# Kernel tuning notes

Measured on AMD Instinct MI355X. Metric: run time of the kernel, lower is better.

The kernel has to match this reference:

```python
import jax, jax.numpy as jnp
import numpy as np

IMG_W, IMG_H = 128, 128
N_PTS = 256
MIN_D, MAX_D = 2.0, 6.0
FOCAL = 1.7320508  # 1/tan(fov/2), fov=60deg (FoVPerspectiveCameras default)
SCALING = 0.1      # scaling_factor default
EPS_EA = 1e-10     # pytorch3d EmissionAbsorptionRaymarcher eps


def setup_inputs() -> dict:
    key = jax.random.key(0)
    k1, k2 = jax.random.split(key)
    image3d = jax.random.uniform(k1, (1, 1, 128, 128, 128), jnp.float32)
    opacity = jax.random.uniform(k2, (1, 1, 128, 128, 128), jnp.float32)
    # row-vector camera convention (pytorch3d): p_cam = p_world @ R + T
    R = jnp.zeros((1, 3, 3), jnp.float32).at[:, jnp.arange(3), jnp.arange(3)].set(1.0)
    T = jnp.zeros((1, 3), jnp.float32).at[:, 2].set(4.0)
    return {"image3d": image3d, "opacity": opacity, "R": R, "T": T}


def _trilinear(vol, pts):
    """vol [C,D,H,W]; pts [N,3] xyz in [-1,1] (x->W, y->H, z->D).
    align_corners=True, zero padding outside. Returns [N,C]."""
    C, D, H, W = vol.shape
    x = (pts[:, 0] + 1.0) * 0.5 * (W - 1)
    y = (pts[:, 1] + 1.0) * 0.5 * (H - 1)
    z = (pts[:, 2] + 1.0) * 0.5 * (D - 1)
    x0 = jnp.floor(x); y0 = jnp.floor(y); z0 = jnp.floor(z)
    wx = x - x0; wy = y - y0; wz = z - z0
    vol_flat = vol.reshape(C, -1)
    out = jnp.zeros((pts.shape[0], C), vol.dtype)
    for dz in (0, 1):
        for dy in (0, 1):
            for dx in (0, 1):
                xi = (x0 + dx).astype(jnp.int32)
                yi = (y0 + dy).astype(jnp.int32)
                zi = (z0 + dz).astype(jnp.int32)
                valid = ((xi >= 0) & (xi < W) & (yi >= 0) & (yi < H)
                         & (zi >= 0) & (zi < D))
                w = ((wx if dx else 1.0 - wx) * (wy if dy else 1.0 - wy)
                     * (wz if dz else 1.0 - wz)) * valid.astype(vol.dtype)
                idx = ((jnp.clip(zi, 0, D - 1) * H + jnp.clip(yi, 0, H - 1)) * W
                       + jnp.clip(xi, 0, W - 1))
                vals = jnp.take(vol_flat, idx, axis=1)  # [C,N]
                out = out + w[:, None] * vals.T
    return out


def _forward(image3d, opacity, R, T):
    B = image3d.shape[0]
    features_vol = jnp.repeat(image3d, 3, axis=1)            # [B,3,D,H,W]
    densities_vol = opacity * SCALING                        # [B,1,D,H,W]
    Dv, Hv, Wv = image3d.shape[2:]
    shape = max(image3d.shape[1], image3d.shape[2])
    voxel = 3.0 / shape
    half_extent = voxel * (jnp.array([Wv, Hv, Dv], jnp.float32) - 1.0) / 2.0

    # NDC pixel grid (pytorch3d: +x left, +y up)
    xs = jnp.linspace(1.0, -1.0, IMG_W)
    ys = jnp.linspace(1.0, -1.0, IMG_H)
    gy, gx = jnp.meshgrid(ys, xs, indexing="ij")             # [H,W]
    dirs_cam = jnp.stack([gx / FOCAL, gy / FOCAL, jnp.ones_like(gx)], -1)  # [H,W,3]
    depths = jnp.linspace(MIN_D, MAX_D, N_PTS)               # [P]

    # row-vector transforms: p_world = (p_cam - T) @ R^T
    origins = jnp.einsum("bi,bji->bj", -T, R)                # camera centers [B,3]
    dirs_world = jnp.einsum("hwi,bji->bhwj", dirs_cam, R)    # [B,H,W,3]
    pts = (origins[:, None, None, None, :]
           + depths[None, None, None, :, None] * dirs_world[:, :, :, None, :])
    local = pts / half_extent                                # [B,H,W,P,3]

    pts_flat = local.reshape(B, -1, 3)
    feats = jax.vmap(_trilinear)(features_vol, pts_flat)
    feats = feats.reshape(B, IMG_H, IMG_W, N_PTS, 3)
    dens = jax.vmap(_trilinear)(densities_vol, pts_flat)
    dens = dens.reshape(B, IMG_H, IMG_W, N_PTS)

    # EmissionAbsorption raymarcher
    cum = jnp.cumprod((1.0 + EPS_EA) - dens, axis=-1)
    absorption = jnp.concatenate([jnp.ones_like(cum[..., :1]), cum[..., :-1]], -1)
    weights = dens * absorption
    feat_out = jnp.sum(weights[..., None] * feats, axis=-2)  # [B,H,W,3]
    opac = 1.0 - jnp.prod(1.0 - dens, axis=-1, keepdims=True)
    rgba = jnp.concatenate([feat_out, opac], axis=-1)        # [B,H,W,4]

    screen = jnp.transpose(rgba, (0, 3, 2, 1))               # permute(0,3,2,1)
    gray = screen[:, :3].mean(axis=1, keepdims=True)         # [B,1,W,H]
    st = (gray - gray.mean()) / (gray.std(ddof=1) + 1e-8)    # standardized
    out = (st - st.min() + 1e-8) / (st.max() - st.min() + 1e-8)  # normalized
    return out


def reference(image3d, opacity, R, T):
    return _forward(image3d, opacity, R, T)
```

## Files before the change

### kernel.cpp

```cpp
#include <hip/hip_runtime.h>
#include <hip/hip_fp16.h>
#include <math.h>


#define FOCAL 1.7320508f

typedef struct __attribute__((packed, aligned(4))) { unsigned int lo, hi; } u2u;

static __device__ __forceinline__ float2 h2f(unsigned int u) {
  __half2 h = *reinterpret_cast<__half2*>(&u);
  return __half22float2(h);
}

__global__ __launch_bounds__(256) void pack_kernel(
    const float4* __restrict__ img, const float4* __restrict__ opa,
    uint4* __restrict__ dst)
{
  const int i = blockIdx.x * 256 + threadIdx.x;
  const float4 f = img[i];
  const float4 o = opa[i];
  const __half2 h0 = __floats2half2_rn(f.x, o.x);
  const __half2 h1 = __floats2half2_rn(f.y, o.y);
  const __half2 h2 = __floats2half2_rn(f.z, o.z);
  const __half2 h3 = __floats2half2_rn(f.w, o.w);
  uint4 r;
  r.x = *(const unsigned int*)&h0;
  r.y = *(const unsigned int*)&h1;
  r.z = *(const unsigned int*)&h2;
  r.w = *(const unsigned int*)&h3;
  dst[i] = r;
}

__global__ __launch_bounds__(1024) void dvr_kernel(
    const unsigned int* __restrict__ vol,
    const float* __restrict__ Rm, const float* __restrict__ Tv,
    float* __restrict__ g, double* __restrict__ bstats,
    unsigned int* __restrict__ counter, float* __restrict__ out)
{
  const int tid  = threadIdx.x;
  const int lane = tid & 63;
  const int seg  = tid >> 6;
  const int B    = blockIdx.x;
  const int b    = ((B & 7) << 5) | (B >> 3);
  const int h    = b >> 1;
  const int w    = ((b & 1) << 6) | lane;

  const float R00=Rm[0], R01=Rm[1], R02=Rm[2];
  const float R10=Rm[3], R11=Rm[4], R12=Rm[5];
  const float R20=Rm[6], R21=Rm[7], R22=Rm[8];
  const float T0=Tv[0], T1=Tv[1], T2=Tv[2];

  const float ox = -(T0*R00 + T1*R01 + T2*R02);
  const float oy = -(T0*R10 + T1*R11 + T2*R12);
  const float oz = -(T0*R20 + T1*R21 + T2*R22);

  const float gx = 1.0f - (2.0f/127.0f) * (float)w;
  const float gy = 1.0f - (2.0f/127.0f) * (float)h;
  const float dcx = gx * (1.0f/FOCAL);
  const float dcy = gy * (1.0f/FOCAL);
  const float dwx = dcx*R00 + dcy*R01 + R02;
  const float dwy = dcx*R10 + dcy*R11 + R12;
  const float dwz = dcx*R20 + dcy*R21 + R22;

  const float s_he = (1.0f/1.48828125f) * 63.5f;
  const float ax = dwx * s_he, bxc = ox * s_he + 63.5f;
  const float ay = dwy * s_he, byc = oy * s_he + 63.5f;
  const float az = dwz * s_he, bzc = oz * s_he + 63.5f;

  const int p0 = seg << 4;

  float lp = 1.0f;
  float accl = 0.0f;

  #pragma unroll 4
  for (int j = 0; j < 16; ++j) {
    const float depth = 2.0f + (4.0f/255.0f) * (float)(p0 + j);
    const float x = bxc + depth * ax;
    const float y = byc + depth * ay;
    const float z = bzc + depth * az;
    const float x0f = floorf(x), y0f = floorf(y), z0f = floorf(z);
    const float wx = x - x0f, wy = y - y0f, wz = z - z0f;
    const int x0 = (int)x0f, y0 = (int)y0f, z0 = (int)z0f;

    float feat = 0.0f, dens = 0.0f;
    if (x0 >= -1 && x0 <= 127 && y0 >= -1 && y0 <= 127 &&
        z0 >= -1 && z0 <= 127) {
      const float fx0 = (x0 >= 0)   ? (1.0f - wx) : 0.0f;
      const float fx1 = (x0 <= 126) ? wx          : 0.0f;
      const float fy0 = (y0 >= 0)   ? (1.0f - wy) : 0.0f;
      const float fy1 = (y0 <= 126) ? wy          : 0.0f;
      const float fz0 = (z0 >= 0)   ? (1.0f - wz) : 0.0f;
      const float fz1 = (z0 <= 126) ? wz          : 0.0f;
      const int iy0 = ((y0 >= 0)   ? y0     : 0)   << 7;
      const int iy1 = ((y0 <= 126) ? y0 + 1 : 127) << 7;
      const int iz0 = ((z0 >= 0)   ? z0     : 0)   << 14;
      const int iz1 = ((z0 <= 126) ? z0 + 1 : 127) << 14;
      const int ixp = (x0 >= 0) ? ((x0 <= 126) ? x0 : 126) : 0;

      const int b00 = iz0 + iy0 + ixp, b01 = iz0 + iy1 + ixp;
      const int b10 = iz1 + iy0 + ixp, b11 = iz1 + iy1 + ixp;
      const float w00 = fz0*fy0, w01 = fz0*fy1, w10 = fz1*fy0, w11 = fz1*fy1;

      const u2u q00 = *(const u2u*)(vol + b00);
      const u2u q01 = *(const u2u*)(vol + b01);
      const u2u q10 = *(const u2u*)(vol + b10);
      const u2u q11 = *(const u2u*)(vol + b11);

      const bool cA = (x0 < 127);
      const bool cB = (x0 >= 0);

      const unsigned int a00 = cA ? q00.lo : q00.hi, b00s = cB ? q00.hi : q00.lo;
      const unsigned int a01 = cA ? q01.lo : q01.hi, b01s = cB ? q01.hi : q01.lo;
      const unsigned int a10 = cA ? q10.lo : q10.hi, b10s = cB ? q10.hi : q10.lo;
      const unsigned int a11 = cA ? q11.lo : q11.hi, b11s = cB ? q11.hi : q11.lo;

      const float2 fa00 = h2f(a00), fb00 = h2f(b00s);
      const float2 fa01 = h2f(a01), fb01 = h2f(b01s);
      const float2 fa10 = h2f(a10), fb10 = h2f(b10s);
      const float2 fa11 = h2f(a11), fb11 = h2f(b11s);

      feat = w00*(fx0*fa00.x + fx1*fb00.x)
           + w01*(fx0*fa01.x + fx1*fb01.x)
           + w10*(fx0*fa10.x + fx1*fb10.x)
           + w11*(fx0*fa11.x + fx1*fb11.x);
      dens = w00*(fx0*fa00.y + fx1*fb00.y)
           + w01*(fx0*fa01.y + fx1*fb01.y)
           + w10*(fx0*fa10.y + fx1*fb10.y)
           + w11*(fx0*fa11.y + fx1*fb11.y);
    }
    const float d = dens * 0.1f;
    accl += feat * d * lp;
    lp   *= (1.0f - d);
  }

  __shared__ float2 slp[16][64];
  slp[seg][lane] = make_float2(accl, lp);
  __syncthreads();

  if (tid < 64) {
    float T = 1.0f, acc = 0.0f;
    #pragma unroll
    for (int s = 0; s < 16; ++s) {
      const float2 v = slp[s][tid];
      acc += v.x * T;
      T *= v.y;
    }
    const int ww = ((b & 1) << 6) | tid;
    g[(ww << 7) + h] = acc;

    double sum = (double)acc;
    double sq  = (double)acc * (double)acc;
    float mn = acc, mx = acc;
    #pragma unroll
    for (int off = 32; off >= 1; off >>= 1) {
      sum += __shfl_xor(sum, off, 64);
      sq  += __shfl_xor(sq,  off, 64);
      mn = fminf(mn, __shfl_xor(mn, off, 64));
      mx = fmaxf(mx, __shfl_xor(mx, off, 64));
    }
    if (tid == 0) {
      bstats[(b << 2) + 0] = sum;
      bstats[(b << 2) + 1] = sq;
      bstats[(b << 2) + 2] = (double)mn;
      bstats[(b << 2) + 3] = (double)mx;
    }
  }
  __syncthreads();

  __shared__ int is_last;
  if (tid == 0) {
    __threadfence();
    const unsigned int old = atomicAdd(counter, 1u);
    const unsigned int base = old - 255u;
    is_last = (base == 0xAAAAAAAAu || base == 0u) ? 1 : 0;
  }
  __syncthreads();
  if (!is_last) return;
  __threadfence();

  double S = 0.0, Q = 0.0;
  float MN = 3.402823466e38f, MX = -3.402823466e38f;
  if (tid < 256) {
    S  = bstats[(tid << 2) + 0];
    Q  = bstats[(tid << 2) + 1];
    MN = (float)bstats[(tid << 2) + 2];
    MX = (float)bstats[(tid << 2) + 3];
  }
  #pragma unroll
  for (int off = 32; off >= 1; off >>= 1) {
    S += __shfl_xor(S, off, 64);
    Q += __shfl_xor(Q, off, 64);
    MN = fminf(MN, __shfl_xor(MN, off, 64));
    MX = fmaxf(MX, __shfl_xor(MX, off, 64));
  }
  __shared__ double rs[16], rq[16];
  __shared__ float rmn[16], rmx[16];
  if (lane == 0) { rs[seg] = S; rq[seg] = Q; rmn[seg] = MN; rmx[seg] = MX; }
  __syncthreads();

  __shared__ float cs[3];
  if (tid == 0) {
    double St = 0.0, Qt = 0.0;
    float MNt = rmn[0], MXt = rmx[0];
    #pragma unroll
    for (int i = 0; i < 4; ++i) {
      St += rs[i]; Qt += rq[i];
      MNt = fminf(MNt, rmn[i]); MXt = fmaxf(MXt, rmx[i]);
    }
    const double mean = St / 16384.0;
    double var = (Qt - 16384.0 * mean * mean) / 16383.0;
    if (var < 0.0) var = 0.0;
    const float sdev = (float)sqrt(var) + 1e-8f;
    cs[0] = MNt;
    cs[1] = 1.0f / sdev;
    cs[2] = 1.0f / ((MXt - MNt) / sdev + 1e-8f);
  }
  __syncthreads();

  const float mnv = cs[0], invs = cs[1], sc = cs[2];
  for (int i = tid; i < 16384; i += 1024) {
    out[i] = ((g[i] - mnv) * invs + 1e-8f) * sc;
  }
}

extern "C" void kernel_launch(void* const* d_in, const int* in_sizes, int n_in,
                              void* d_out, int out_size, void* d_ws, size_t ws_size,
                              hipStream_t stream) {
  const float* img = (const float*)d_in[0];
  const float* opa = (const float*)d_in[1];
  const float* Rm  = (const float*)d_in[2];
  const float* Tv  = (const float*)d_in[3];
  float* out = (float*)d_out;

  char* wsb = (char*)d_ws;
  float*        g       = (float*)wsb;
  double*       bstats  = (double*)(wsb + 65536);
  unsigned int* counter = (unsigned int*)(wsb + 65536 + 8192);
  unsigned int* vol     = (unsigned int*)(wsb + (1 << 20));

  pack_kernel<<<2048, 256, 0, stream>>>((const float4*)img, (const float4*)opa,
                                        (uint4*)vol);
  dvr_kernel<<<256, 1024, 0, stream>>>(vol, Rm, Tv, g, bstats, counter, out);
}
```

Measured before the change: 98.75 us.

## Split each ray group's samples across two blocks and merge partial transmittance

Doubles the grid from 256 to 512 blocks by splitting each ray's 256 samples into two halves handled by separate blocks. Each block writes a partial (accumulated color, transmittance) pair, and the second block of each pair to finish composites both halves via a per-group atomic counter. The aim is better occupancy and load spread across the GPU's compute units, since 256 blocks underfill the device. In exchange it adds a second atomic handoff with extra global round trips, relies on workspace counters that cycle between calls, and changes the launch_bounds hint.

```diff
diff --git a/kernel.cpp b/kernel.cpp
--- a/kernel.cpp
+++ b/kernel.cpp
@@ -31,19 +31,23 @@
   dst[i] = r;
 }
 
-__global__ __launch_bounds__(1024) void dvr_kernel(
+__global__ __launch_bounds__(1024, 8) void dvr_kernel(
     const unsigned int* __restrict__ vol,
     const float* __restrict__ Rm, const float* __restrict__ Tv,
     float* __restrict__ g, double* __restrict__ bstats,
-    unsigned int* __restrict__ counter, float* __restrict__ out)
+    unsigned int* __restrict__ done, unsigned int* __restrict__ pc,
+    float2* __restrict__ part, float* __restrict__ out)
 {
   const int tid  = threadIdx.x;
   const int lane = tid & 63;
-  const int seg  = tid >> 6;
+  const int wseg = tid >> 6;
   const int B    = blockIdx.x;
-  const int b    = ((B & 7) << 5) | (B >> 3);
-  const int h    = b >> 1;
-  const int w    = ((b & 1) << 6) | lane;
+  const int logical = ((B & 7) << 6) | (B >> 3);
+  const int group = logical >> 1;
+  const int half  = logical & 1;
+  const int h  = group >> 1;
+  const int wq = group & 1;
+  const int w  = (wq << 6) | lane;
 
   const float R00=Rm[0], R01=Rm[1], R02=Rm[2];
   const float R10=Rm[3], R11=Rm[4], R12=Rm[5];
@@ -67,13 +71,13 @@
   const float ay = dwy * s_he, byc = oy * s_he + 63.5f;
   const float az = dwz * s_he, bzc = oz * s_he + 63.5f;
 
-  const int p0 = seg << 4;
+  const int p0 = (half << 7) + (wseg << 3);
 
   float lp = 1.0f;
   float accl = 0.0f;
 
   #pragma unroll 4
-  for (int j = 0; j < 16; ++j) {
+  for (int j = 0; j < 8; ++j) {
     const float depth = 2.0f + (4.0f/255.0f) * (float)(p0 + j);
     const float x = bxc + depth * ax;
     const float y = byc + depth * ay;
@@ -134,19 +138,35 @@
   }
 
   __shared__ float2 slp[16][64];
-  slp[seg][lane] = make_float2(accl, lp);
-  __syncthreads();
-
+  slp[wseg][lane] = make_float2(accl, lp);
+  __syncthreads();
+
+  float accP = 0.0f, TP = 1.0f;
   if (tid < 64) {
-    float T = 1.0f, acc = 0.0f;
     #pragma unroll
     for (int s = 0; s < 16; ++s) {
       const float2 v = slp[s][tid];
-      acc += v.x * T;
-      T *= v.y;
-    }
-    const int ww = ((b & 1) << 6) | tid;
-    g[(ww << 7) + h] = acc;
+      accP += v.x * TP;
+      TP *= v.y;
+    }
+    part[(group << 7) + (half << 6) + tid] = make_float2(accP, TP);
+  }
+
+  __shared__ int flag1, flag2;
+  if (tid == 0) {
+    __threadfence();
+    const unsigned int old = atomicAdd(&pc[group], 1u);
+    const unsigned int base = old - 1u;
+    flag1 = (base == 0xAAAAAAAAu || base == 0u) ? 1 : 0;
+  }
+  __syncthreads();
+  if (!flag1) return;
+  __threadfence();
+
+  if (tid < 64) {
+    const float2 oth = part[(group << 7) + ((half ^ 1) << 6) + tid];
+    const float acc = half ? (oth.x + oth.y * accP) : (accP + TP * oth.x);
+    g[(w << 7) + h] = acc;
 
     double sum = (double)acc;
     double sq  = (double)acc * (double)acc;
@@ -159,23 +179,21 @@
       mx = fmaxf(mx, __shfl_xor(mx, off, 64));
     }
     if (tid == 0) {
-      bstats[(b << 2) + 0] = sum;
-      bstats[(b << 2) + 1] = sq;
-      bstats[(b << 2) + 2] = (double)mn;
-      bstats[(b << 2) + 3] = (double)mx;
-    }
-  }
-  __syncthreads();
-
-  __shared__ int is_last;
+      bstats[(group << 2) + 0] = sum;
+      bstats[(group << 2) + 1] = sq;
+      bstats[(group << 2) + 2] = (double)mn;
+      bstats[(group << 2) + 3] = (double)mx;
+    }
+  }
+
   if (tid == 0) {
     __threadfence();
-    const unsigned int old = atomicAdd(counter, 1u);
+    const unsigned int old = atomicAdd(done, 1u);
     const unsigned int base = old - 255u;
-    is_last = (base == 0xAAAAAAAAu || base == 0u) ? 1 : 0;
-  }
-  __syncthreads();
-  if (!is_last) return;
+    flag2 = (base == 0xAAAAAAAAu || base == 0u) ? 1 : 0;
+  }
+  __syncthreads();
+  if (!flag2) return;
   __threadfence();
 
   double S = 0.0, Q = 0.0;
@@ -195,7 +213,7 @@
   }
   __shared__ double rs[16], rq[16];
   __shared__ float rmn[16], rmx[16];
-  if (lane == 0) { rs[seg] = S; rq[seg] = Q; rmn[seg] = MN; rmx[seg] = MX; }
+  if (lane == 0) { rs[wseg] = S; rq[wseg] = Q; rmn[wseg] = MN; rmx[wseg] = MX; }
   __syncthreads();
 
   __shared__ float cs[3];
@@ -235,10 +253,13 @@
   char* wsb = (char*)d_ws;
   float*        g       = (float*)wsb;
   double*       bstats  = (double*)(wsb + 65536);
-  unsigned int* counter = (unsigned int*)(wsb + 65536 + 8192);
+  unsigned int* done    = (unsigned int*)(wsb + 73728);
+  unsigned int* pc      = (unsigned int*)(wsb + 73792);
+  float2*       part    = (float2*)(wsb + 131072);
   unsigned int* vol     = (unsigned int*)(wsb + (1 << 20));
 
   pack_kernel<<<2048, 256, 0, stream>>>((const float4*)img, (const float4*)opa,
                                         (uint4*)vol);
-  dvr_kernel<<<256, 1024, 0, stream>>>(vol, Rm, Tv, g, bstats, counter, out);
-}
+  dvr_kernel<<<512, 1024, 0, stream>>>(vol, Rm, Tv, g, bstats, done, pc,
+                                       part, out);
+}
```

After: 163.9 us. 1.66x slower.
